# Performance work log

Hardware: AMD Instinct MI355X
Metric: run time of the kernel (lower is better)

Reference implementation:

```python
import jax, jax.numpy as jnp
import numpy as np

EPS_BN = 1e-5
B, N, H = 8, 256, 64


def setup_inputs() -> dict:
    key = jax.random.key(0)
    ks = jax.random.split(key, 10)
    s = 1.0 / np.sqrt(H)
    return {
        "x": jax.random.normal(ks[0], (B, N, H), dtype=jnp.float32),
        "e": jax.random.normal(ks[1], (B, N, N, H), dtype=jnp.float32),
        # EdgeFeatures linears (torch Linear: y = x @ W.T + b, W:(out,in))
        "Ue_W": jax.random.uniform(ks[2], (H, H), jnp.float32, -s, s),
        "Ue_b": jax.random.uniform(ks[3], (H,), jnp.float32, -s, s),
        "Ve_W": jax.random.uniform(ks[4], (H, H), jnp.float32, -s, s),
        "Ve_b": jax.random.uniform(ks[5], (H,), jnp.float32, -s, s),
        # NodeFeatures linears
        "Un_W": jax.random.uniform(ks[6], (H, H), jnp.float32, -s, s),
        "Un_b": jax.random.uniform(ks[7], (H,), jnp.float32, -s, s),
        "Vn_W": jax.random.uniform(ks[8], (H, H), jnp.float32, -s, s),
        "Vn_b": jax.random.uniform(ks[9], (H,), jnp.float32, -s, s),
        # BatchNorm affine params (track_running_stats=False -> batch stats)
        "bne_g": jnp.ones((H,), jnp.float32),
        "bne_b": jnp.zeros((H,), jnp.float32),
        "bnn_g": jnp.ones((H,), jnp.float32),
        "bnn_b": jnp.zeros((H,), jnp.float32),
    }


def _bn(t, gamma, beta, axes):
    # PyTorch BatchNorm with track_running_stats=False: biased batch var
    mean = jnp.mean(t, axis=axes, keepdims=True)
    var = jnp.mean(jnp.square(t - mean), axis=axes, keepdims=True)
    return (t - mean) * jax.lax.rsqrt(var + EPS_BN) * gamma + beta


def _forward(x, e, Ue_W, Ue_b, Ve_W, Ve_b, Un_W, Un_b, Vn_W, Vn_b,
             bne_g, bne_b, bnn_g, bnn_b):
    # EdgeFeatures: e_tmp = U(e) + V(x)_i + V(x)_j
    Ue = jnp.einsum('bijh,oh->bijo', e, Ue_W) + Ue_b          # (B,N,N,H)
    Vxe = x @ Ve_W.T + Ve_b                                    # (B,N,H)
    e_tmp = Ue + Vxe[:, :, None, :] + Vxe[:, None, :, :]       # (B,N,N,H)
    edge_gate = jax.nn.sigmoid(e_tmp)
    # NodeFeatures (aggregation='sum'): x_tmp = U(x) + sum_j gate_ij * V(x)_j
    Ux = x @ Un_W.T + Un_b                                     # (B,N,H)
    Vxn = x @ Vn_W.T + Vn_b                                    # (B,N,H)
    x_tmp = Ux + jnp.sum(edge_gate * Vxn[:, None, :, :], axis=2)
    # BatchNorm (edge: per-channel over B,N,N; node: over B,N), ReLU, residual
    e_bn = _bn(e_tmp, bne_g, bne_b, axes=(0, 1, 2))
    x_bn = _bn(x_tmp, bnn_g, bnn_b, axes=(0, 1))
    x_new = jax.nn.relu(x_bn) + x
    e_new = jax.nn.relu(e_bn) + e
    return x_new, e_new


def reference(x, e, Ue_W, Ue_b, Ve_W, Ve_b, Un_W, Un_b, Vn_W, Vn_b,
              bne_g, bne_b, bnn_g, bnn_b):
    return _forward(x, e, Ue_W, Ue_b, Ve_W, Ve_b, Un_W, Un_b, Vn_W, Vn_b,
                    bne_g, bne_b, bnn_g, bnn_b)
```

## Files before the change

### kernel.cpp

```cpp
#include <hip/hip_runtime.h>
#include <cstddef>
#include <cstdint>

constexpr int Bv = 8, Nv = 256, Hv = 64;
constexpr int ROWS = Bv * Nv;
constexpr float INV_EDGE_CNT = 1.0f / (8.0f * 256.0f * 256.0f);
constexpr float INV_NODE_CNT = 1.0f / 2048.0f;
constexpr float EPSBN = 1e-5f;

constexpr size_t WS_VXE  = 0;
constexpr size_t WS_VXN  = 131072;
constexpr size_t WS_UX   = 262144;
constexpr size_t WS_AGG  = 393216;
constexpr size_t WS_ESUM = 524288;
constexpr size_t WS_ESQ  = 524352;
constexpr size_t WS_PART = 524416;

typedef __bf16 bf16x8 __attribute__((ext_vector_type(8)));
typedef float  f32x4  __attribute__((ext_vector_type(4)));

__device__ __forceinline__ float4 ld4(const float* p) {
  return *reinterpret_cast<const float4*>(p);
}

__device__ __forceinline__ bf16x8 cvt8(float4 a, float4 b) {
  bf16x8 r;
  r[0] = (__bf16)a.x; r[1] = (__bf16)a.y; r[2] = (__bf16)a.z; r[3] = (__bf16)a.w;
  r[4] = (__bf16)b.x; r[5] = (__bf16)b.y; r[6] = (__bf16)b.z; r[7] = (__bf16)b.w;
  return r;
}

__device__ __forceinline__ void loadA(float4 A[4], const float* eTile,
                                      int j0, int r16, int g) {
  const float* ep = eTile + (size_t)(j0 + r16) * 64 + 8 * g;
  A[0] = ld4(ep);      A[1] = ld4(ep + 4);
  A[2] = ld4(ep + 32); A[3] = ld4(ep + 36);
}

__device__ __forceinline__ void load_tile_G(const float* eTile, int w, int lane,
                                            int tt, float4 G[4]) {
#pragma unroll
  for (int k = 0; k < 4; ++k) {
    const int m  = k * 64 + lane;
    const int rl = m >> 4;
    const int pp = m & 15;
    const int cc = pp ^ (rl & 7);
    G[k] = ld4(eTile + (size_t)(w * 64 + tt * 16 + rl) * 64 + cc * 4);
  }
}

__device__ __forceinline__ void write_tile_L(float* myBuf, int lane, int s,
                                             const float4 G[4]) {
#pragma unroll
  for (int k = 0; k < 4; ++k)
    *(float4*)(myBuf + s * 1024 + k * 256 + lane * 4) = G[k];
}

#define DOT4(acc, a, b) \
  acc = fmaf((a).x, (b).x, fmaf((a).y, (b).y, fmaf((a).z, (b).z, fmaf((a).w, (b).w, acc))))

__global__ __launch_bounds__(128) void k_lin(
    const float* __restrict__ x,
    const float* __restrict__ VeW, const float* __restrict__ Veb,
    const float* __restrict__ UnW, const float* __restrict__ Unb,
    const float* __restrict__ VnW, const float* __restrict__ Vnb,
    float* __restrict__ ws)
{
  const int idx = blockIdx.x * 128 + threadIdx.x;
  const int r  = idx >> 4;
  const int tg = idx & 15;
  const int t  = tg >> 2, g = tg & 3;
  const int c0 = t * 16 + g * 4;

  const float4* x4 = (const float4*)(x + (size_t)r * 64);
  float a1[4] = {}, a2[4] = {}, a3[4] = {};
#pragma unroll
  for (int h = 0; h < 16; ++h) {
    float4 xv = x4[h];
#pragma unroll
    for (int cc = 0; cc < 4; ++cc) {
      float4 w1 = ld4(VeW + (size_t)(c0 + cc) * 64 + h * 4); DOT4(a1[cc], xv, w1);
      float4 w2 = ld4(UnW + (size_t)(c0 + cc) * 64 + h * 4); DOT4(a2[cc], xv, w2);
      float4 w3 = ld4(VnW + (size_t)(c0 + cc) * 64 + h * 4); DOT4(a3[cc], xv, w3);
    }
  }

  const int b = r >> 8, jt = (r >> 4) & 15, r16 = r & 15;
  const size_t pidx = ((size_t)((b * 16 + jt) * 4 + t)) * 256 + (g * 16 + r16) * 4;
  *(float4*)(&ws[WS_VXE + pidx]) =
      make_float4(a1[0] + Veb[c0], a1[1] + Veb[c0 + 1], a1[2] + Veb[c0 + 2], a1[3] + Veb[c0 + 3]);
  *(float4*)(&ws[WS_VXN + pidx]) =
      make_float4(a3[0] + Vnb[c0], a3[1] + Vnb[c0 + 1], a3[2] + Vnb[c0 + 2], a3[3] + Vnb[c0 + 3]);
  *(float4*)(&ws[WS_UX + (size_t)r * 64 + c0]) =
      make_float4(a2[0] + Unb[c0], a2[1] + Unb[c0 + 1], a2[2] + Unb[c0 + 2], a2[3] + Unb[c0 + 3]);
}

__global__ __launch_bounds__(256, 3) void k_edgeA(
    const float* __restrict__ e,
    const float* __restrict__ UeW, const float* __restrict__ Ueb,
    float* __restrict__ ws)
{
  __shared__ float redL[3 * 256];

  const int tid  = threadIdx.x;
  const int lane = tid & 63;
  const int w    = tid >> 6;
  const int bi   = blockIdx.x;
  const int b    = bi >> 8;
  const int r16  = lane & 15;
  const int g    = lane >> 4;

  const float* eTile = e + (size_t)bi * (Nv * Hv);
  const float* VXEP = ws + WS_VXE;
  const float* VXNP = ws + WS_VXN;

  bf16x8 wF0[4], wF1[4];
#pragma unroll
  for (int t = 0; t < 4; ++t) {
    const float* wrow = UeW + (size_t)(t * 16 + r16) * 64 + 8 * g;
    wF0[t] = cvt8(ld4(wrow),      ld4(wrow + 4));
    wF1[t] = cvt8(ld4(wrow + 32), ld4(wrow + 36));
  }

  const int jti = (bi >> 4) & 15, r16i = bi & 15;
  float uv[4][4];
#pragma unroll
  for (int t = 0; t < 4; ++t) {
    float4 ub = ld4(Ueb + t * 16 + 4 * g);
    float4 vi = ld4(VXEP + ((size_t)((b * 16 + jti) * 4 + t)) * 256 + (g * 16 + r16i) * 4);
    uv[t][0] = ub.x + vi.x; uv[t][1] = ub.y + vi.y;
    uv[t][2] = ub.z + vi.z; uv[t][3] = ub.w + vi.w;
  }

  float4 A0[4], A1[4];
  loadA(A0, eTile, w * 64 + 0 * 16, r16, g);
  loadA(A1, eTile, w * 64 + 1 * 16, r16, g);

  float sS[4][4] = {}, sQ[4][4] = {}, sA[4][4] = {};

#pragma unroll
  for (int p = 0; p < 4; ++p) {
    const size_t pb = (size_t)((b * 16 + (w * 4 + p)) * 4);
    float4 vj4[4], vn4[4];
#pragma unroll
    for (int t = 0; t < 4; ++t) {
      vj4[t] = ld4(VXEP + (pb + t) * 256 + lane * 4);
      vn4[t] = ld4(VXNP + (pb + t) * 256 + lane * 4);
    }

    float4* As = (p & 1) ? A1 : A0;
    bf16x8 aF0 = cvt8(As[0], As[1]);
    bf16x8 aF1 = cvt8(As[2], As[3]);
    if (p < 2) loadA(As, eTile, w * 64 + (p + 2) * 16, r16, g);

    f32x4 acc[4];
#pragma unroll
    for (int t = 0; t < 4; ++t) {
      f32x4 z = {0.f, 0.f, 0.f, 0.f};
      acc[t] = __builtin_amdgcn_mfma_f32_16x16x32_bf16(wF0[t], aF0, z, 0, 0, 0);
      acc[t] = __builtin_amdgcn_mfma_f32_16x16x32_bf16(wF1[t], aF1, acc[t], 0, 0, 0);
    }

#pragma unroll
    for (int t = 0; t < 4; ++t) {
      float vj[4] = {vj4[t].x, vj4[t].y, vj4[t].z, vj4[t].w};
      float vn[4] = {vn4[t].x, vn4[t].y, vn4[t].z, vn4[t].w};
#pragma unroll
      for (int r = 0; r < 4; ++r) {
        float tv = acc[t][r] + uv[t][r] + vj[r];
        sS[t][r] += tv;
        sQ[t][r]  = fmaf(tv, tv, sQ[t][r]);
        float sg  = __builtin_amdgcn_rcpf(1.0f + __expf(-tv));
        sA[t][r]  = fmaf(sg, vn[r], sA[t][r]);
      }
    }
  }

#pragma unroll
  for (int t = 0; t < 4; ++t)
#pragma unroll
    for (int r = 0; r < 4; ++r) {
#pragma unroll
      for (int m = 1; m < 16; m <<= 1) {
        sS[t][r] += __shfl_xor(sS[t][r], m);
        sQ[t][r] += __shfl_xor(sQ[t][r], m);
        sA[t][r] += __shfl_xor(sA[t][r], m);
      }
    }

  if (r16 == 0) {
#pragma unroll
    for (int t = 0; t < 4; ++t) {
      const int cb = w * 64 + t * 16 + 4 * g;
      *(float4*)(&redL[cb])       = make_float4(sA[t][0], sA[t][1], sA[t][2], sA[t][3]);
      *(float4*)(&redL[256 + cb]) = make_float4(sS[t][0], sS[t][1], sS[t][2], sS[t][3]);
      *(float4*)(&redL[512 + cb]) = make_float4(sQ[t][0], sQ[t][1], sQ[t][2], sQ[t][3]);
    }
  }
  __syncthreads();
  if (tid < 64) {
    const int c = tid;
    float a  = redL[c]       + redL[64 + c]        + redL[128 + c]       + redL[192 + c];
    ws[WS_AGG + (size_t)bi * 64 + c] = a;
    float s  = redL[256 + c] + redL[256 + 64 + c]  + redL[256 + 128 + c] + redL[256 + 192 + c];
    float qv = redL[512 + c] + redL[512 + 64 + c]  + redL[512 + 128 + c] + redL[512 + 192 + c];
    ws[WS_PART + (size_t)bi * 128 + c]      = s;
    ws[WS_PART + (size_t)bi * 128 + 64 + c] = qv;
  }
}

__global__ __launch_bounds__(256) void k_node(
    const float* __restrict__ x,
    const float* __restrict__ bnng, const float* __restrict__ bnnb,
    const float* __restrict__ bneg, const float* __restrict__ bneb,
    float* __restrict__ ws, float* __restrict__ xOut)
{
  const int c = blockIdx.x;
  const int tid = threadIdx.x;
  __shared__ float ss[4], qq[4];
  const int w = tid >> 6;

  float S = 0.f, Q = 0.f;
#pragma unroll
  for (int k = 0; k < 8; ++k) {
    const size_t row = (size_t)(tid + 256 * k) * 128;
    S += ws[WS_PART + row + c];
    Q += ws[WS_PART + row + 64 + c];
  }
#pragma unroll
  for (int m = 1; m < 64; m <<= 1) {
    S += __shfl_xor(S, m);
    Q += __shfl_xor(Q, m);
  }
  if ((tid & 63) == 0) { ss[w] = S; qq[w] = Q; }
  __syncthreads();
  if (tid == 0) {
    float Se = ss[0] + ss[1] + ss[2] + ss[3];
    float Qe = qq[0] + qq[1] + qq[2] + qq[3];
    float mean = Se * INV_EDGE_CNT;
    float var  = Qe * INV_EDGE_CNT - mean * mean;
    float sc = rsqrtf(var + EPSBN) * bneg[c];
    ws[WS_ESUM + c] = sc;
    ws[WS_ESQ  + c] = bneb[c] - mean * sc;
  }
  __syncthreads();

  const float* Ux  = ws + WS_UX;
  const float* agg = ws + WS_AGG;

  float v[8];
  float s = 0.f, q = 0.f;
#pragma unroll
  for (int k = 0; k < 8; ++k) {
    int r = tid + 256 * k;
    float t = Ux[(size_t)r * 64 + c] + agg[(size_t)r * 64 + c];
    v[k] = t;
    s += t;
    q = fmaf(t, t, q);
  }
#pragma unroll
  for (int m = 1; m < 64; m <<= 1) {
    s += __shfl_xor(s, m);
    q += __shfl_xor(q, m);
  }
  if ((tid & 63) == 0) { ss[w] = s; qq[w] = q; }
  __syncthreads();
  float Sn = ss[0] + ss[1] + ss[2] + ss[3];
  float Qn = qq[0] + qq[1] + qq[2] + qq[3];
  float mean = Sn * INV_NODE_CNT;
  float var  = Qn * INV_NODE_CNT - mean * mean;
  float scv = rsqrtf(var + EPSBN) * bnng[c];
  float shv = bnnb[c] - mean * scv;
#pragma unroll
  for (int k = 0; k < 8; ++k) {
    int r = tid + 256 * k;
    float y = fmaf(v[k], scv, shv);
    xOut[(size_t)r * 64 + c] = fmaxf(y, 0.f) + x[(size_t)r * 64 + c];
  }
}

__global__ __launch_bounds__(256) void k_edgeC(
    const float* __restrict__ e,
    const float* __restrict__ UeW, const float* __restrict__ Ueb,
    const float* __restrict__ ws, float* __restrict__ eOut)
{
  __shared__ __align__(16) float eL[4 * 2048];
  __shared__ __align__(16) __bf16 wLds[4096];

  const int tid  = threadIdx.x;
  const int lane = tid & 63;
  const int w    = tid >> 6;
  const int bi   = blockIdx.x;
  const int b    = bi >> 8;
  const int r16  = lane & 15;
  const int g    = lane >> 4;
  const int sw   = r16 & 7;

  const float* eTile = e + (size_t)bi * (Nv * Hv);
  float* myBuf = &eL[w * 2048];
  float* oTile = eOut + (size_t)bi * (Nv * Hv);

#pragma unroll
  for (int k = 0; k < 2; ++k) {
    const int m = tid * 2 + k;
    const int c = m >> 3, p = m & 7;
    float4 lo = ld4(UeW + (size_t)c * 64 + p * 8);
    float4 hi = ld4(UeW + (size_t)c * 64 + p * 8 + 4);
    *(bf16x8*)(&wLds[(size_t)c * 64 + (size_t)(p ^ (c & 7)) * 8]) = cvt8(lo, hi);
  }

  const float* VXEP = ws + WS_VXE;
  const int jti = (bi >> 4) & 15, r16i = bi & 15;
  float4 ueb4[4], vxei4[4], sc4[4], sh4[4];
#pragma unroll
  for (int t = 0; t < 4; ++t) {
    ueb4[t]  = ld4(Ueb + t * 16 + 4 * g);
    vxei4[t] = ld4(VXEP + ((size_t)((b * 16 + jti) * 4 + t)) * 256 + (g * 16 + r16i) * 4);
    sc4[t]   = ld4(ws + WS_ESUM + t * 16 + 4 * g);
    sh4[t]   = ld4(ws + WS_ESQ  + t * 16 + 4 * g);
  }

  float4 Ga[4], Gb[4];
  float4 Pj[2][4];
  load_tile_G(eTile, w, lane, 0, Ga);
  load_tile_G(eTile, w, lane, 1, Gb);
  {
    const size_t pb0 = (size_t)((b * 16 + (w * 4 + 0)) * 4);
#pragma unroll
    for (int t = 0; t < 4; ++t)
      Pj[0][t] = ld4(VXEP + (pb0 + t) * 256 + lane * 4);
  }
  __syncthreads();
  write_tile_L(myBuf, lane, 0, Ga);
  write_tile_L(myBuf, lane, 1, Gb);

#pragma unroll
  for (int p = 0; p < 4; ++p) {
    bf16x8 wF0[4], wF1[4];
#pragma unroll
    for (int t = 0; t < 4; ++t) {
      const int wr = (16 * t + r16) * 64;
      wF0[t] = *(const bf16x8*)(&wLds[wr + ((g ^ sw) << 3)]);
      wF1[t] = *(const bf16x8*)(&wLds[wr + (((4 + g) ^ sw) << 3)]);
    }
    const float* rbase = myBuf + (p & 1) * 1024 + r16 * 64;
    float4 f0 = ld4(rbase + (((2 * g)     ^ sw) << 2));
    float4 f1 = ld4(rbase + (((2 * g + 1) ^ sw) << 2));
    float4 f2 = ld4(rbase + ((((2 * g)     ^ sw) + 8) << 2));
    float4 f3 = ld4(rbase + ((((2 * g + 1) ^ sw) + 8) << 2));
    bf16x8 aF0 = cvt8(f0, f1);
    bf16x8 aF1 = cvt8(f2, f3);
    float4 res4[4];
#pragma unroll
    for (int t = 0; t < 4; ++t)
      res4[t] = ld4(rbase + (((4 * t + g) ^ sw) << 2));

    if (p < 3) {
      const size_t pbn = (size_t)((b * 16 + (w * 4 + p + 1)) * 4);
#pragma unroll
      for (int t = 0; t < 4; ++t)
        Pj[(p + 1) & 1][t] = ld4(VXEP + (pbn + t) * 256 + lane * 4);
    }
    if (p < 2) load_tile_G(eTile, w, lane, p + 2, (p & 1) ? Gb : Ga);

    f32x4 acc[4];
#pragma unroll
    for (int t = 0; t < 4; ++t) {
      f32x4 z = {0.f, 0.f, 0.f, 0.f};
      acc[t] = __builtin_amdgcn_mfma_f32_16x16x32_bf16(wF0[t], aF0, z, 0, 0, 0);
      acc[t] = __builtin_amdgcn_mfma_f32_16x16x32_bf16(wF1[t], aF1, acc[t], 0, 0, 0);
    }

    const int j = w * 64 + p * 16 + r16;
#pragma unroll
    for (int t = 0; t < 4; ++t) {
      float vj[4] = {Pj[p & 1][t].x, Pj[p & 1][t].y, Pj[p & 1][t].z, Pj[p & 1][t].w};
      float rs[4] = {res4[t].x, res4[t].y, res4[t].z, res4[t].w};
      float ub[4] = {ueb4[t].x, ueb4[t].y, ueb4[t].z, ueb4[t].w};
      float vi[4] = {vxei4[t].x, vxei4[t].y, vxei4[t].z, vxei4[t].w};
      float sc[4] = {sc4[t].x, sc4[t].y, sc4[t].z, sc4[t].w};
      float sh[4] = {sh4[t].x, sh4[t].y, sh4[t].z, sh4[t].w};
      float out[4];
#pragma unroll
      for (int r = 0; r < 4; ++r) {
        float tv = acc[t][r] + ub[r] + vi[r] + vj[r];
        float y  = fmaf(tv, sc[r], sh[r]);
        out[r] = fmaxf(y, 0.f) + rs[r];
      }
      *(float4*)(oTile + (size_t)j * 64 + t * 16 + 4 * g) =
          make_float4(out[0], out[1], out[2], out[3]);
    }

    if (p < 2) write_tile_L(myBuf, lane, p & 1, (p & 1) ? Gb : Ga);
    __builtin_amdgcn_sched_barrier(0);
  }
}

extern "C" void kernel_launch(void* const* d_in, const int* in_sizes, int n_in,
                              void* d_out, int out_size, void* d_ws, size_t ws_size,
                              hipStream_t stream)
{
  const float* x    = (const float*)d_in[0];
  const float* e    = (const float*)d_in[1];
  const float* UeW  = (const float*)d_in[2];
  const float* Ueb  = (const float*)d_in[3];
  const float* VeW  = (const float*)d_in[4];
  const float* Veb  = (const float*)d_in[5];
  const float* UnW  = (const float*)d_in[6];
  const float* Unb  = (const float*)d_in[7];
  const float* VnW  = (const float*)d_in[8];
  const float* Vnb  = (const float*)d_in[9];
  const float* bneg = (const float*)d_in[10];
  const float* bneb = (const float*)d_in[11];
  const float* bnng = (const float*)d_in[12];
  const float* bnnb = (const float*)d_in[13];

  float* ws   = (float*)d_ws;
  float* xOut = (float*)d_out;
  float* eOut = (float*)d_out + (size_t)ROWS * Hv;

  k_lin<<<256, 128, 0, stream>>>(x, VeW, Veb, UnW, Unb, VnW, Vnb, ws);
  k_edgeA<<<ROWS, 256, 0, stream>>>(e, UeW, Ueb, ws);
  k_node<<<Hv, 256, 0, stream>>>(x, bnng, bnnb, bneg, bneb, ws, xOut);
  k_edgeC<<<ROWS, 256, 0, stream>>>(e, UeW, Ueb, ws, eOut);
}
```

Baseline: 122.4 us.

## Process four edge rows per block in edge kernels to amortize setup

Both edge kernels now handle four consecutive (b,i) rows per block, launching 512 blocks instead of 2048. Weight fragment loads, the LDS weight staging and bias loads are done once per block and reused across the four rows. BN partial sums are accumulated across the rows, so the partial buffer shrinks and the node kernel reads fewer rows. In exchange there is less parallelism (512 blocks), a lower occupancy hint, and extra syncthreads per row. Prefetch no longer overlaps across row boundaries.

```diff
diff --git a/kernel.cpp b/kernel.cpp
--- a/kernel.cpp
+++ b/kernel.cpp
@@ -4,6 +4,7 @@
 
 constexpr int Bv = 8, Nv = 256, Hv = 64;
 constexpr int ROWS = Bv * Nv;
+constexpr int EBLK = 512;
 constexpr float INV_EDGE_CNT = 1.0f / (8.0f * 256.0f * 256.0f);
 constexpr float INV_NODE_CNT = 1.0f / 2048.0f;
 constexpr float EPSBN = 1e-5f;
@@ -95,7 +96,7 @@
       make_float4(a2[0] + Unb[c0], a2[1] + Unb[c0 + 1], a2[2] + Unb[c0 + 2], a2[3] + Unb[c0 + 3]);
 }
 
-__global__ __launch_bounds__(256, 3) void k_edgeA(
+__global__ __launch_bounds__(256, 2) void k_edgeA4(
     const float* __restrict__ e,
     const float* __restrict__ UeW, const float* __restrict__ Ueb,
     float* __restrict__ ws)
@@ -105,12 +106,11 @@
   const int tid  = threadIdx.x;
   const int lane = tid & 63;
   const int w    = tid >> 6;
-  const int bi   = blockIdx.x;
-  const int b    = bi >> 8;
+  const int bi0  = blockIdx.x * 4;
+  const int b    = bi0 >> 8;
   const int r16  = lane & 15;
   const int g    = lane >> 4;
 
-  const float* eTile = e + (size_t)bi * (Nv * Hv);
   const float* VXEP = ws + WS_VXE;
   const float* VXNP = ws + WS_VXN;
 
@@ -122,58 +122,91 @@
     wF1[t] = cvt8(ld4(wrow + 32), ld4(wrow + 36));
   }
 
-  const int jti = (bi >> 4) & 15, r16i = bi & 15;
-  float uv[4][4];
-#pragma unroll
-  for (int t = 0; t < 4; ++t) {
-    float4 ub = ld4(Ueb + t * 16 + 4 * g);
-    float4 vi = ld4(VXEP + ((size_t)((b * 16 + jti) * 4 + t)) * 256 + (g * 16 + r16i) * 4);
-    uv[t][0] = ub.x + vi.x; uv[t][1] = ub.y + vi.y;
-    uv[t][2] = ub.z + vi.z; uv[t][3] = ub.w + vi.w;
-  }
-
-  float4 A0[4], A1[4];
-  loadA(A0, eTile, w * 64 + 0 * 16, r16, g);
-  loadA(A1, eTile, w * 64 + 1 * 16, r16, g);
-
-  float sS[4][4] = {}, sQ[4][4] = {}, sA[4][4] = {};
-
-#pragma unroll
-  for (int p = 0; p < 4; ++p) {
-    const size_t pb = (size_t)((b * 16 + (w * 4 + p)) * 4);
-    float4 vj4[4], vn4[4];
+  float4 ueb4[4];
+#pragma unroll
+  for (int t = 0; t < 4; ++t) ueb4[t] = ld4(Ueb + t * 16 + 4 * g);
+
+  float sSg[4][4] = {}, sQg[4][4] = {};
+
+#pragma unroll
+  for (int q = 0; q < 4; ++q) {
+    const int bi = bi0 + q;
+    const float* eTile = e + (size_t)bi * (Nv * Hv);
+
+    const int jti = (bi >> 4) & 15, r16i = bi & 15;
+    float uv[4][4];
 #pragma unroll
     for (int t = 0; t < 4; ++t) {
-      vj4[t] = ld4(VXEP + (pb + t) * 256 + lane * 4);
-      vn4[t] = ld4(VXNP + (pb + t) * 256 + lane * 4);
-    }
-
-    float4* As = (p & 1) ? A1 : A0;
-    bf16x8 aF0 = cvt8(As[0], As[1]);
-    bf16x8 aF1 = cvt8(As[2], As[3]);
-    if (p < 2) loadA(As, eTile, w * 64 + (p + 2) * 16, r16, g);
-
-    f32x4 acc[4];
-#pragma unroll
-    for (int t = 0; t < 4; ++t) {
-      f32x4 z = {0.f, 0.f, 0.f, 0.f};
-      acc[t] = __builtin_amdgcn_mfma_f32_16x16x32_bf16(wF0[t], aF0, z, 0, 0, 0);
-      acc[t] = __builtin_amdgcn_mfma_f32_16x16x32_bf16(wF1[t], aF1, acc[t], 0, 0, 0);
-    }
-
-#pragma unroll
-    for (int t = 0; t < 4; ++t) {
-      float vj[4] = {vj4[t].x, vj4[t].y, vj4[t].z, vj4[t].w};
-      float vn[4] = {vn4[t].x, vn4[t].y, vn4[t].z, vn4[t].w};
+      float4 vi = ld4(VXEP + ((size_t)((b * 16 + jti) * 4 + t)) * 256 + (g * 16 + r16i) * 4);
+      uv[t][0] = ueb4[t].x + vi.x; uv[t][1] = ueb4[t].y + vi.y;
+      uv[t][2] = ueb4[t].z + vi.z; uv[t][3] = ueb4[t].w + vi.w;
+    }
+
+    float4 A0[4], A1[4];
+    loadA(A0, eTile, w * 64 + 0 * 16, r16, g);
+    loadA(A1, eTile, w * 64 + 1 * 16, r16, g);
+
+    float sA[4][4] = {};
+
+#pragma unroll
+    for (int p = 0; p < 4; ++p) {
+      const size_t pb = (size_t)((b * 16 + (w * 4 + p)) * 4);
+      float4 vj4[4], vn4[4];
+#pragma unroll
+      for (int t = 0; t < 4; ++t) {
+        vj4[t] = ld4(VXEP + (pb + t) * 256 + lane * 4);
+        vn4[t] = ld4(VXNP + (pb + t) * 256 + lane * 4);
+      }
+
+      float4* As = (p & 1) ? A1 : A0;
+      bf16x8 aF0 = cvt8(As[0], As[1]);
+      bf16x8 aF1 = cvt8(As[2], As[3]);
+      if (p < 2) loadA(As, eTile, w * 64 + (p + 2) * 16, r16, g);
+
+      f32x4 acc[4];
+#pragma unroll
+      for (int t = 0; t < 4; ++t) {
+        f32x4 z = {0.f, 0.f, 0.f, 0.f};
+        acc[t] = __builtin_amdgcn_mfma_f32_16x16x32_bf16(wF0[t], aF0, z, 0, 0, 0);
+        acc[t] = __builtin_amdgcn_mfma_f32_16x16x32_bf16(wF1[t], aF1, acc[t], 0, 0, 0);
+      }
+
+#pragma unroll
+      for (int t = 0; t < 4; ++t) {
+        float vj[4] = {vj4[t].x, vj4[t].y, vj4[t].z, vj4[t].w};
+        float vn[4] = {vn4[t].x, vn4[t].y, vn4[t].z, vn4[t].w};
+#pragma unroll
+        for (int r = 0; r < 4; ++r) {
+          float tv = acc[t][r] + uv[t][r] + vj[r];
+          sSg[t][r] += tv;
+          sQg[t][r]  = fmaf(tv, tv, sQg[t][r]);
+          float sg   = __builtin_amdgcn_rcpf(1.0f + __expf(-tv));
+          sA[t][r]   = fmaf(sg, vn[r], sA[t][r]);
+        }
+      }
+    }
+
+#pragma unroll
+    for (int t = 0; t < 4; ++t)
 #pragma unroll
       for (int r = 0; r < 4; ++r) {
-        float tv = acc[t][r] + uv[t][r] + vj[r];
-        sS[t][r] += tv;
-        sQ[t][r]  = fmaf(tv, tv, sQ[t][r]);
-        float sg  = __builtin_amdgcn_rcpf(1.0f + __expf(-tv));
-        sA[t][r]  = fmaf(sg, vn[r], sA[t][r]);
-      }
-    }
+#pragma unroll
+        for (int m = 1; m < 16; m <<= 1)
+          sA[t][r] += __shfl_xor(sA[t][r], m);
+      }
+    if (r16 == 0) {
+#pragma unroll
+      for (int t = 0; t < 4; ++t)
+        *(float4*)(&redL[w * 64 + t * 16 + 4 * g]) =
+            make_float4(sA[t][0], sA[t][1], sA[t][2], sA[t][3]);
+    }
+    __syncthreads();
+    if (tid < 64) {
+      const int c = tid;
+      ws[WS_AGG + (size_t)bi * 64 + c] =
+          redL[c] + redL[64 + c] + redL[128 + c] + redL[192 + c];
+    }
+    __syncthreads();
   }
 
 #pragma unroll
@@ -182,30 +215,25 @@
     for (int r = 0; r < 4; ++r) {
 #pragma unroll
       for (int m = 1; m < 16; m <<= 1) {
-        sS[t][r] += __shfl_xor(sS[t][r], m);
-        sQ[t][r] += __shfl_xor(sQ[t][r], m);
-        sA[t][r] += __shfl_xor(sA[t][r], m);
-      }
-    }
-
+        sSg[t][r] += __shfl_xor(sSg[t][r], m);
+        sQg[t][r] += __shfl_xor(sQg[t][r], m);
+      }
+    }
   if (r16 == 0) {
 #pragma unroll
     for (int t = 0; t < 4; ++t) {
       const int cb = w * 64 + t * 16 + 4 * g;
-      *(float4*)(&redL[cb])       = make_float4(sA[t][0], sA[t][1], sA[t][2], sA[t][3]);
-      *(float4*)(&redL[256 + cb]) = make_float4(sS[t][0], sS[t][1], sS[t][2], sS[t][3]);
-      *(float4*)(&redL[512 + cb]) = make_float4(sQ[t][0], sQ[t][1], sQ[t][2], sQ[t][3]);
+      *(float4*)(&redL[cb])       = make_float4(sSg[t][0], sSg[t][1], sSg[t][2], sSg[t][3]);
+      *(float4*)(&redL[256 + cb]) = make_float4(sQg[t][0], sQg[t][1], sQg[t][2], sQg[t][3]);
     }
   }
   __syncthreads();
   if (tid < 64) {
     const int c = tid;
-    float a  = redL[c]       + redL[64 + c]        + redL[128 + c]       + redL[192 + c];
-    ws[WS_AGG + (size_t)bi * 64 + c] = a;
-    float s  = redL[256 + c] + redL[256 + 64 + c]  + redL[256 + 128 + c] + redL[256 + 192 + c];
-    float qv = redL[512 + c] + redL[512 + 64 + c]  + redL[512 + 128 + c] + redL[512 + 192 + c];
-    ws[WS_PART + (size_t)bi * 128 + c]      = s;
-    ws[WS_PART + (size_t)bi * 128 + 64 + c] = qv;
+    ws[WS_PART + (size_t)blockIdx.x * 128 + c] =
+        redL[c] + redL[64 + c] + redL[128 + c] + redL[192 + c];
+    ws[WS_PART + (size_t)blockIdx.x * 128 + 64 + c] =
+        redL[256 + c] + redL[256 + 64 + c] + redL[256 + 128 + c] + redL[256 + 192 + c];
   }
 }
 
@@ -222,7 +250,7 @@
 
   float S = 0.f, Q = 0.f;
 #pragma unroll
-  for (int k = 0; k < 8; ++k) {
+  for (int k = 0; k < 2; ++k) {
     const size_t row = (size_t)(tid + 256 * k) * 128;
     S += ws[WS_PART + row + c];
     Q += ws[WS_PART + row + 64 + c];
@@ -279,7 +307,7 @@
   }
 }
 
-__global__ __launch_bounds__(256) void k_edgeC(
+__global__ __launch_bounds__(256, 2) void k_edgeC4(
     const float* __restrict__ e,
     const float* __restrict__ UeW, const float* __restrict__ Ueb,
     const float* __restrict__ ws, float* __restrict__ eOut)
@@ -290,15 +318,14 @@
   const int tid  = threadIdx.x;
   const int lane = tid & 63;
   const int w    = tid >> 6;
-  const int bi   = blockIdx.x;
-  const int b    = bi >> 8;
+  const int bi0  = blockIdx.x * 4;
+  const int b    = bi0 >> 8;
   const int r16  = lane & 15;
   const int g    = lane >> 4;
   const int sw   = r16 & 7;
 
-  const float* eTile = e + (size_t)bi * (Nv * Hv);
   float* myBuf = &eL[w * 2048];
-  float* oTile = eOut + (size_t)bi * (Nv * Hv);
+  const float* VXEP = ws + WS_VXE;
 
 #pragma unroll
   for (int k = 0; k < 2; ++k) {
@@ -309,90 +336,101 @@
     *(bf16x8*)(&wLds[(size_t)c * 64 + (size_t)(p ^ (c & 7)) * 8]) = cvt8(lo, hi);
   }
 
-  const float* VXEP = ws + WS_VXE;
-  const int jti = (bi >> 4) & 15, r16i = bi & 15;
-  float4 ueb4[4], vxei4[4], sc4[4], sh4[4];
+  float4 ueb4[4], sc4[4], sh4[4];
 #pragma unroll
   for (int t = 0; t < 4; ++t) {
-    ueb4[t]  = ld4(Ueb + t * 16 + 4 * g);
-    vxei4[t] = ld4(VXEP + ((size_t)((b * 16 + jti) * 4 + t)) * 256 + (g * 16 + r16i) * 4);
-    sc4[t]   = ld4(ws + WS_ESUM + t * 16 + 4 * g);
-    sh4[t]   = ld4(ws + WS_ESQ  + t * 16 + 4 * g);
-  }
-
-  float4 Ga[4], Gb[4];
-  float4 Pj[2][4];
-  load_tile_G(eTile, w, lane, 0, Ga);
-  load_tile_G(eTile, w, lane, 1, Gb);
-  {
-    const size_t pb0 = (size_t)((b * 16 + (w * 4 + 0)) * 4);
+    ueb4[t] = ld4(Ueb + t * 16 + 4 * g);
+    sc4[t]  = ld4(ws + WS_ESUM + t * 16 + 4 * g);
+    sh4[t]  = ld4(ws + WS_ESQ  + t * 16 + 4 * g);
+  }
+
+  __syncthreads();
+  bf16x8 wF0[4], wF1[4];
+#pragma unroll
+  for (int t = 0; t < 4; ++t) {
+    const int wr = (16 * t + r16) * 64;
+    wF0[t] = *(const bf16x8*)(&wLds[wr + ((g ^ sw) << 3)]);
+    wF1[t] = *(const bf16x8*)(&wLds[wr + (((4 + g) ^ sw) << 3)]);
+  }
+
+#pragma unroll
+  for (int q = 0; q < 4; ++q) {
+    const int bi = bi0 + q;
+    const float* eTile = e + (size_t)bi * (Nv * Hv);
+    float* oTile = eOut + (size_t)bi * (Nv * Hv);
+
+    const int jti = (bi >> 4) & 15, r16i = bi & 15;
+    float4 vxei4[4];
 #pragma unroll
     for (int t = 0; t < 4; ++t)
-      Pj[0][t] = ld4(VXEP + (pb0 + t) * 256 + lane * 4);
-  }
-  __syncthreads();
-  write_tile_L(myBuf, lane, 0, Ga);
-  write_tile_L(myBuf, lane, 1, Gb);
-
-#pragma unroll
-  for (int p = 0; p < 4; ++p) {
-    bf16x8 wF0[4], wF1[4];
-#pragma unroll
-    for (int t = 0; t < 4; ++t) {
-      const int wr = (16 * t + r16) * 64;
-      wF0[t] = *(const bf16x8*)(&wLds[wr + ((g ^ sw) << 3)]);
-      wF1[t] = *(const bf16x8*)(&wLds[wr + (((4 + g) ^ sw) << 3)]);
-    }
-    const float* rbase = myBuf + (p & 1) * 1024 + r16 * 64;
-    float4 f0 = ld4(rbase + (((2 * g)     ^ sw) << 2));
-    float4 f1 = ld4(rbase + (((2 * g + 1) ^ sw) << 2));
-    float4 f2 = ld4(rbase + ((((2 * g)     ^ sw) + 8) << 2));
-    float4 f3 = ld4(rbase + ((((2 * g + 1) ^ sw) + 8) << 2));
-    bf16x8 aF0 = cvt8(f0, f1);
-    bf16x8 aF1 = cvt8(f2, f3);
-    float4 res4[4];
-#pragma unroll
-    for (int t = 0; t < 4; ++t)
-      res4[t] = ld4(rbase + (((4 * t + g) ^ sw) << 2));
-
-    if (p < 3) {
-      const size_t pbn = (size_t)((b * 16 + (w * 4 + p + 1)) * 4);
+      vxei4[t] = ld4(VXEP + ((size_t)((b * 16 + jti) * 4 + t)) * 256 + (g * 16 + r16i) * 4);
+
+    float4 Ga[4], Gb[4];
+    float4 Pj[2][4];
+    load_tile_G(eTile, w, lane, 0, Ga);
+    load_tile_G(eTile, w, lane, 1, Gb);
+    {
+      const size_t pb0 = (size_t)((b * 16 + (w * 4 + 0)) * 4);
 #pragma unroll
       for (int t = 0; t < 4; ++t)
-        Pj[(p + 1) & 1][t] = ld4(VXEP + (pbn + t) * 256 + lane * 4);
-    }
-    if (p < 2) load_tile_G(eTile, w, lane, p + 2, (p & 1) ? Gb : Ga);
-
-    f32x4 acc[4];
-#pragma unroll
-    for (int t = 0; t < 4; ++t) {
-      f32x4 z = {0.f, 0.f, 0.f, 0.f};
-      acc[t] = __builtin_amdgcn_mfma_f32_16x16x32_bf16(wF0[t], aF0, z, 0, 0, 0);
-      acc[t] = __builtin_amdgcn_mfma_f32_16x16x32_bf16(wF1[t], aF1, acc[t], 0, 0, 0);
-    }
-
-    const int j = w * 64 + p * 16 + r16;
-#pragma unroll
-    for (int t = 0; t < 4; ++t) {
-      float vj[4] = {Pj[p & 1][t].x, Pj[p & 1][t].y, Pj[p & 1][t].z, Pj[p & 1][t].w};
-      float rs[4] = {res4[t].x, res4[t].y, res4[t].z, res4[t].w};
-      float ub[4] = {ueb4[t].x, ueb4[t].y, ueb4[t].z, ueb4[t].w};
-      float vi[4] = {vxei4[t].x, vxei4[t].y, vxei4[t].z, vxei4[t].w};
-      float sc[4] = {sc4[t].x, sc4[t].y, sc4[t].z, sc4[t].w};
-      float sh[4] = {sh4[t].x, sh4[t].y, sh4[t].z, sh4[t].w};
-      float out[4];
-#pragma unroll
-      for (int r = 0; r < 4; ++r) {
-        float tv = acc[t][r] + ub[r] + vi[r] + vj[r];
-        float y  = fmaf(tv, sc[r], sh[r]);
-        out[r] = fmaxf(y, 0.f) + rs[r];
-      }
-      *(float4*)(oTile + (size_t)j * 64 + t * 16 + 4 * g) =
-          make_float4(out[0], out[1], out[2], out[3]);
-    }
-
-    if (p < 2) write_tile_L(myBuf, lane, p & 1, (p & 1) ? Gb : Ga);
-    __builtin_amdgcn_sched_barrier(0);
+        Pj[0][t] = ld4(VXEP + (pb0 + t) * 256 + lane * 4);
+    }
+    write_tile_L(myBuf, lane, 0, Ga);
+    write_tile_L(myBuf, lane, 1, Gb);
+
+#pragma unroll
+    for (int p = 0; p < 4; ++p) {
+      const float* rbase = myBuf + (p & 1) * 1024 + r16 * 64;
+      float4 f0 = ld4(rbase + (((2 * g)     ^ sw) << 2));
+      float4 f1 = ld4(rbase + (((2 * g + 1) ^ sw) << 2));
+      float4 f2 = ld4(rbase + ((((2 * g)     ^ sw) + 8) << 2));
+      float4 f3 = ld4(rbase + ((((2 * g + 1) ^ sw) + 8) << 2));
+      bf16x8 aF0 = cvt8(f0, f1);
+      bf16x8 aF1 = cvt8(f2, f3);
+      float4 res4[4];
+#pragma unroll
+      for (int t = 0; t < 4; ++t)
+        res4[t] = ld4(rbase + (((4 * t + g) ^ sw) << 2));
+
+      if (p < 3) {
+        const size_t pbn = (size_t)((b * 16 + (w * 4 + p + 1)) * 4);
+#pragma unroll
+        for (int t = 0; t < 4; ++t)
+          Pj[(p + 1) & 1][t] = ld4(VXEP + (pbn + t) * 256 + lane * 4);
+      }
+      if (p < 2) load_tile_G(eTile, w, lane, p + 2, (p & 1) ? Gb : Ga);
+
+      f32x4 acc[4];
+#pragma unroll
+      for (int t = 0; t < 4; ++t) {
+        f32x4 z = {0.f, 0.f, 0.f, 0.f};
+        acc[t] = __builtin_amdgcn_mfma_f32_16x16x32_bf16(wF0[t], aF0, z, 0, 0, 0);
+        acc[t] = __builtin_amdgcn_mfma_f32_16x16x32_bf16(wF1[t], aF1, acc[t], 0, 0, 0);
+      }
+
+      const int j = w * 64 + p * 16 + r16;
+#pragma unroll
+      for (int t = 0; t < 4; ++t) {
+        float vj[4] = {Pj[p & 1][t].x, Pj[p & 1][t].y, Pj[p & 1][t].z, Pj[p & 1][t].w};
+        float rs[4] = {res4[t].x, res4[t].y, res4[t].z, res4[t].w};
+        float ub[4] = {ueb4[t].x, ueb4[t].y, ueb4[t].z, ueb4[t].w};
+        float vi[4] = {vxei4[t].x, vxei4[t].y, vxei4[t].z, vxei4[t].w};
+        float sc[4] = {sc4[t].x, sc4[t].y, sc4[t].z, sc4[t].w};
+        float sh[4] = {sh4[t].x, sh4[t].y, sh4[t].z, sh4[t].w};
+        float out[4];
+#pragma unroll
+        for (int r = 0; r < 4; ++r) {
+          float tv = acc[t][r] + ub[r] + vi[r] + vj[r];
+          float y  = fmaf(tv, sc[r], sh[r]);
+          out[r] = fmaxf(y, 0.f) + rs[r];
+        }
+        *(float4*)(oTile + (size_t)j * 64 + t * 16 + 4 * g) =
+            make_float4(out[0], out[1], out[2], out[3]);
+      }
+
+      if (p < 2) write_tile_L(myBuf, lane, p & 1, (p & 1) ? Gb : Ga);
+      __builtin_amdgcn_sched_barrier(0);
+    }
   }
 }
 
@@ -420,7 +458,7 @@
   float* eOut = (float*)d_out + (size_t)ROWS * Hv;
 
   k_lin<<<256, 128, 0, stream>>>(x, VeW, Veb, UnW, Unb, VnW, Vnb, ws);
-  k_edgeA<<<ROWS, 256, 0, stream>>>(e, UeW, Ueb, ws);
+  k_edgeA4<<<EBLK, 256, 0, stream>>>(e, UeW, Ueb, ws);
   k_node<<<Hv, 256, 0, stream>>>(x, bnng, bnnb, bneg, bneb, ws, xOut);
-  k_edgeC<<<ROWS, 256, 0, stream>>>(e, UeW, Ueb, ws, eOut);
-}
+  k_edgeC4<<<EBLK, 256, 0, stream>>>(e, UeW, Ueb, ws, eOut);
+}
```

After: 192.9 us. +57.6%, slower.

## Stage edge tiles and bf16 weights through swizzled LDS in edge kernel

Applied to the files above, without the earlier changes.

The edge kernel now loads each e tile with a coalesced, XOR-swizzled global pattern and writes it into a per-wave double-buffered LDS region. MFMA operands are then read from LDS instead of directly from strided global rows. The Ue weight matrix is converted to bf16 once per block into swizzled LDS rather than every lane loading and converting its own fragment. This aims for better global load coalescing and less redundant weight traffic, at the cost of about 40KB of LDS per block, which may limit occupancy. The launch-bounds occupancy hint is also dropped, and the reduction scratch reuses the staging buffer.

```diff
diff --git a/kernel.cpp b/kernel.cpp
--- a/kernel.cpp
+++ b/kernel.cpp
@@ -28,13 +28,6 @@
   r[0] = (__bf16)a.x; r[1] = (__bf16)a.y; r[2] = (__bf16)a.z; r[3] = (__bf16)a.w;
   r[4] = (__bf16)b.x; r[5] = (__bf16)b.y; r[6] = (__bf16)b.z; r[7] = (__bf16)b.w;
   return r;
-}
-
-__device__ __forceinline__ void loadA(float4 A[4], const float* eTile,
-                                      int j0, int r16, int g) {
-  const float* ep = eTile + (size_t)(j0 + r16) * 64 + 8 * g;
-  A[0] = ld4(ep);      A[1] = ld4(ep + 4);
-  A[2] = ld4(ep + 32); A[3] = ld4(ep + 36);
 }
 
 __device__ __forceinline__ void load_tile_G(const float* eTile, int w, int lane,
@@ -95,12 +88,13 @@
       make_float4(a2[0] + Unb[c0], a2[1] + Unb[c0 + 1], a2[2] + Unb[c0 + 2], a2[3] + Unb[c0 + 3]);
 }
 
-__global__ __launch_bounds__(256, 3) void k_edgeA(
+__global__ __launch_bounds__(256) void k_edgeA(
     const float* __restrict__ e,
     const float* __restrict__ UeW, const float* __restrict__ Ueb,
     float* __restrict__ ws)
 {
-  __shared__ float redL[3 * 256];
+  __shared__ __align__(16) float eL[4 * 2048];
+  __shared__ __align__(16) __bf16 wLds[4096];
 
   const int tid  = threadIdx.x;
   const int lane = tid & 63;
@@ -109,18 +103,22 @@
   const int b    = bi >> 8;
   const int r16  = lane & 15;
   const int g    = lane >> 4;
+  const int sw   = r16 & 7;
 
   const float* eTile = e + (size_t)bi * (Nv * Hv);
+  float* myBuf = &eL[w * 2048];
+
+#pragma unroll
+  for (int k = 0; k < 2; ++k) {
+    const int m = tid * 2 + k;
+    const int c = m >> 3, p = m & 7;
+    float4 lo = ld4(UeW + (size_t)c * 64 + p * 8);
+    float4 hi = ld4(UeW + (size_t)c * 64 + p * 8 + 4);
+    *(bf16x8*)(&wLds[(size_t)c * 64 + (size_t)(p ^ (c & 7)) * 8]) = cvt8(lo, hi);
+  }
+
   const float* VXEP = ws + WS_VXE;
   const float* VXNP = ws + WS_VXN;
-
-  bf16x8 wF0[4], wF1[4];
-#pragma unroll
-  for (int t = 0; t < 4; ++t) {
-    const float* wrow = UeW + (size_t)(t * 16 + r16) * 64 + 8 * g;
-    wF0[t] = cvt8(ld4(wrow),      ld4(wrow + 4));
-    wF1[t] = cvt8(ld4(wrow + 32), ld4(wrow + 36));
-  }
 
   const int jti = (bi >> 4) & 15, r16i = bi & 15;
   float uv[4][4];
@@ -132,9 +130,20 @@
     uv[t][2] = ub.z + vi.z; uv[t][3] = ub.w + vi.w;
   }
 
-  float4 A0[4], A1[4];
-  loadA(A0, eTile, w * 64 + 0 * 16, r16, g);
-  loadA(A1, eTile, w * 64 + 1 * 16, r16, g);
+  float4 Ga[4], Gb[4];
+  load_tile_G(eTile, w, lane, 0, Ga);
+  load_tile_G(eTile, w, lane, 1, Gb);
+  __syncthreads();
+  write_tile_L(myBuf, lane, 0, Ga);
+  write_tile_L(myBuf, lane, 1, Gb);
+
+  bf16x8 wF0[4], wF1[4];
+#pragma unroll
+  for (int t = 0; t < 4; ++t) {
+    const int wr = (16 * t + r16) * 64;
+    wF0[t] = *(const bf16x8*)(&wLds[wr + ((g ^ sw) << 3)]);
+    wF1[t] = *(const bf16x8*)(&wLds[wr + (((4 + g) ^ sw) << 3)]);
+  }
 
   float sS[4][4] = {}, sQ[4][4] = {}, sA[4][4] = {};
 
@@ -148,10 +157,15 @@
       vn4[t] = ld4(VXNP + (pb + t) * 256 + lane * 4);
     }
 
-    float4* As = (p & 1) ? A1 : A0;
-    bf16x8 aF0 = cvt8(As[0], As[1]);
-    bf16x8 aF1 = cvt8(As[2], As[3]);
-    if (p < 2) loadA(As, eTile, w * 64 + (p + 2) * 16, r16, g);
+    const float* rbase = myBuf + (p & 1) * 1024 + r16 * 64;
+    float4 f0 = ld4(rbase + (((2 * g)     ^ sw) << 2));
+    float4 f1 = ld4(rbase + (((2 * g + 1) ^ sw) << 2));
+    float4 f2 = ld4(rbase + ((((2 * g)     ^ sw) + 8) << 2));
+    float4 f3 = ld4(rbase + ((((2 * g + 1) ^ sw) + 8) << 2));
+    bf16x8 aF0 = cvt8(f0, f1);
+    bf16x8 aF1 = cvt8(f2, f3);
+
+    if (p < 2) load_tile_G(eTile, w, lane, p + 2, (p & 1) ? Gb : Ga);
 
     f32x4 acc[4];
 #pragma unroll
@@ -174,6 +188,9 @@
         sA[t][r]  = fmaf(sg, vn[r], sA[t][r]);
       }
     }
+
+    if (p < 2) write_tile_L(myBuf, lane, p & 1, (p & 1) ? Gb : Ga);
+    __builtin_amdgcn_sched_barrier(0);
   }
 
 #pragma unroll
@@ -191,19 +208,19 @@
   if (r16 == 0) {
 #pragma unroll
     for (int t = 0; t < 4; ++t) {
-      const int cb = w * 64 + t * 16 + 4 * g;
-      *(float4*)(&redL[cb])       = make_float4(sA[t][0], sA[t][1], sA[t][2], sA[t][3]);
-      *(float4*)(&redL[256 + cb]) = make_float4(sS[t][0], sS[t][1], sS[t][2], sS[t][3]);
-      *(float4*)(&redL[512 + cb]) = make_float4(sQ[t][0], sQ[t][1], sQ[t][2], sQ[t][3]);
+      const int cb = t * 16 + 4 * g;
+      *(float4*)(&myBuf[cb])       = make_float4(sA[t][0], sA[t][1], sA[t][2], sA[t][3]);
+      *(float4*)(&myBuf[256 + cb]) = make_float4(sS[t][0], sS[t][1], sS[t][2], sS[t][3]);
+      *(float4*)(&myBuf[512 + cb]) = make_float4(sQ[t][0], sQ[t][1], sQ[t][2], sQ[t][3]);
     }
   }
   __syncthreads();
   if (tid < 64) {
     const int c = tid;
-    float a  = redL[c]       + redL[64 + c]        + redL[128 + c]       + redL[192 + c];
+    float a  = eL[c]       + eL[2048 + c]       + eL[4096 + c]       + eL[6144 + c];
     ws[WS_AGG + (size_t)bi * 64 + c] = a;
-    float s  = redL[256 + c] + redL[256 + 64 + c]  + redL[256 + 128 + c] + redL[256 + 192 + c];
-    float qv = redL[512 + c] + redL[512 + 64 + c]  + redL[512 + 128 + c] + redL[512 + 192 + c];
+    float s  = eL[256 + c] + eL[2048 + 256 + c] + eL[4096 + 256 + c] + eL[6144 + 256 + c];
+    float qv = eL[512 + c] + eL[2048 + 512 + c] + eL[4096 + 512 + c] + eL[6144 + 512 + c];
     ws[WS_PART + (size_t)bi * 128 + c]      = s;
     ws[WS_PART + (size_t)bi * 128 + 64 + c] = qv;
   }
```

After: 113.0 us. 7.7% less time.
